# Optimization experiments

Hardware: AMD Instinct MI355X
Metric: run time of the kernel (lower is better)

Reference implementation:

```python
import jax, jax.numpy as jnp
import numpy as np

DIM = 1024
NUM_HEADS = 16
HEAD_DIM = DIM // NUM_HEADS
B, S = 2, 2048


def setup_inputs() -> dict:
    key = jax.random.key(0)
    ks = jax.random.split(key, 12)
    sc = 1.0 / np.sqrt(DIM)
    inp = {
        'x': jax.random.normal(ks[0], (B, S, DIM), dtype=jnp.float32),
        'Wq': jax.random.normal(ks[1], (DIM, DIM), dtype=jnp.float32) * sc,
        'bq': jnp.zeros((DIM,), dtype=jnp.float32),
        'Wk': jax.random.normal(ks[2], (DIM, DIM), dtype=jnp.float32) * sc,
        'bk': jnp.zeros((DIM,), dtype=jnp.float32),
        'Wv': jax.random.normal(ks[3], (DIM, DIM), dtype=jnp.float32) * sc,
        'bv': jnp.zeros((DIM,), dtype=jnp.float32),
        'Wg1': jax.random.normal(ks[4], (DIM, DIM // 2), dtype=jnp.float32) * sc,
        'bg1': jnp.zeros((DIM // 2,), dtype=jnp.float32),
        'Wg2': jax.random.normal(ks[5], (DIM // 2, NUM_HEADS), dtype=jnp.float32) * (1.0 / np.sqrt(DIM // 2)),
        'bg2': jnp.zeros((NUM_HEADS,), dtype=jnp.float32),
        'Wo': jax.random.normal(ks[6], (DIM, DIM), dtype=jnp.float32) * sc,
        'bo': jnp.zeros((DIM,), dtype=jnp.float32),
    }
    return inp


def reference(x, Wq, bq, Wk, bk, Wv, bv, Wg1, bg1, Wg2, bg2, Wo, bo):
    b, s, dim = x.shape
    h, d = NUM_HEADS, HEAD_DIM
    # QKV projections -> (b, h, s, d)
    q = (x @ Wq + bq).reshape(b, s, h, d).transpose(0, 2, 1, 3)
    k = (x @ Wk + bk).reshape(b, s, h, d).transpose(0, 2, 1, 3)
    v = (x @ Wv + bv).reshape(b, s, h, d).transpose(0, 2, 1, 3)
    # raw attention scores (b, h, q, k)
    scores = jnp.einsum('bhqd,bhkd->bhqk', q, k) / np.sqrt(d)
    # superposition gate: per-(batch, token) softmax over heads -> (b, s, h)
    gate = jax.nn.softmax(jnp.tanh(x @ Wg1 + bg1) @ Wg2 + bg2, axis=-1)
    gate = gate.transpose(0, 2, 1)[..., None]  # (b, h, s, 1) -- per-query scale
    scores = scores * gate
    probs = jax.nn.softmax(scores, axis=-1)
    # dropout is identity at inference
    attended = jnp.einsum('bhqk,bhkd->bhqd', probs, v)
    attended = attended.transpose(0, 2, 1, 3).reshape(b, s, dim)
    return attended @ Wo + bo
```

## Files before the change

### kernel.cpp

```cpp
#include <hip/hip_runtime.h>
#include <math.h>

#define DIM    1024
#define NHEADS 16
#define HDIM   64
#define BATCH  2
#define SEQ    2048
#define TOK    (BATCH * SEQ)

typedef unsigned short ushort;
typedef __attribute__((ext_vector_type(8))) short  short8;
typedef __attribute__((ext_vector_type(4))) float  f32x4;
typedef __attribute__((ext_vector_type(4))) unsigned short us4;

__device__ __forceinline__ ushort f2bf(float f) {
    unsigned u = __float_as_uint(f);
    u += 0x7fffu + ((u >> 16) & 1u);
    return (ushort)(u >> 16);
}
__device__ __forceinline__ float bf2f(ushort h) {
    return __uint_as_float(((unsigned)h) << 16);
}

__device__ __forceinline__ void gload16(const void* g, void* lds) {
    __builtin_amdgcn_global_load_lds(
        (const __attribute__((address_space(1))) unsigned int*)g,
        (__attribute__((address_space(3))) unsigned int*)lds, 16, 0, 0);
}

__global__ __launch_bounds__(256) void split_hl(
    const float* __restrict__ in, ushort* __restrict__ hi, ushort* __restrict__ lo)
{
    const int i = blockIdx.x * 256 + threadIdx.x;
    float4 v = ((const float4*)in)[i];
    us4 h, l;
    h.x = f2bf(v.x); l.x = f2bf(v.x - bf2f(h.x));
    h.y = f2bf(v.y); l.y = f2bf(v.y - bf2f(h.y));
    h.z = f2bf(v.z); l.z = f2bf(v.z - bf2f(h.z));
    h.w = f2bf(v.w); l.w = f2bf(v.w - bf2f(h.w));
    ((us4*)hi)[i] = h;
    ((us4*)lo)[i] = l;
}

__device__ __forceinline__ void tsplit_body(
    const float* __restrict__ in, ushort* __restrict__ hiT, ushort* __restrict__ loT,
    int K, int N, int k0, int n0)
{
    __shared__ float t[32][33];
    const int x = threadIdx.x & 31, y = threadIdx.x >> 5;
#pragma unroll
    for (int r = 0; r < 4; ++r)
        t[y + r * 8][x] = in[(size_t)(k0 + y + r * 8) * N + n0 + x];
    __syncthreads();
#pragma unroll
    for (int r = 0; r < 4; ++r) {
        const int row = y + r * 8;
        const float v = t[x][row];
        const ushort h = f2bf(v);
        const size_t o = (size_t)(n0 + row) * K + k0 + x;
        hiT[o] = h;
        loT[o] = f2bf(v - bf2f(h));
    }
}

__global__ __launch_bounds__(256) void wsplitT4(
    const float* __restrict__ W0, const float* __restrict__ W1,
    const float* __restrict__ W2, const float* __restrict__ W3,
    ushort* __restrict__ hiT, ushort* __restrict__ loT)
{
    const int z = blockIdx.z;
    const float* in = (z == 0) ? W0 : (z == 1) ? W1 : (z == 2) ? W2 : W3;
    tsplit_body(in, hiT + (size_t)z * DIM * DIM, loT + (size_t)z * DIM * DIM,
                DIM, DIM, blockIdx.y * 32, blockIdx.x * 32);
}

__global__ __launch_bounds__(256) void wsplitT1(
    const float* __restrict__ in, ushort* __restrict__ hiT, ushort* __restrict__ loT,
    int K, int N)
{
    tsplit_body(in, hiT, loT, K, N, blockIdx.y * 32, blockIdx.x * 32);
}

__global__ __launch_bounds__(256) void vtrans(
    const ushort* __restrict__ vh, ushort* __restrict__ vT)
{
    __shared__ ushort t[32][33];
    const int bh = blockIdx.z;
    const int s0 = blockIdx.x * 32, d0 = blockIdx.y * 32;
    const int x = threadIdx.x & 31, y = threadIdx.x >> 5;
    const ushort* src = vh + (size_t)bh * SEQ * HDIM;
    ushort* dst = vT + (size_t)bh * HDIM * SEQ;
#pragma unroll
    for (int r = 0; r < 4; ++r)
        t[y + r * 8][x] = src[(size_t)(s0 + y + r * 8) * HDIM + d0 + x];
    __syncthreads();
#pragma unroll
    for (int r = 0; r < 4; ++r)
        dst[(size_t)(d0 + y + r * 8) * SEQ + s0 + x] = t[x][y + r * 8];
}

template<int MREP>
__device__ __forceinline__ void mgemm_core(
    const ushort* __restrict__ Ahi, const ushort* __restrict__ Alo,
    const ushort* __restrict__ BThi, const ushort* __restrict__ BTlo,
    const float* __restrict__ bias, int act, int store,
    float* __restrict__ Cf, ushort* __restrict__ Ch, ushort* __restrict__ Cl,
    int ldc, int row0, int col0, ushort* ldsA, ushort* ldsB)
{
    const int tid  = threadIdx.x;
    const int lane = tid & 63;
    const int wid  = tid >> 6;
    const int wr   = wid >> 1;
    const int wc   = wid & 1;
    const int l15  = lane & 15;
    const int l4   = lane >> 4;

    f32x4 acc[MREP][4];
#pragma unroll
    for (int m = 0; m < MREP; ++m)
#pragma unroll
        for (int n = 0; n < 4; ++n) acc[m][n] = (f32x4){0.f, 0.f, 0.f, 0.f};

    const int trow = wid * 8 + (lane >> 3);
    const int swz  = ((lane & 7) ^ (lane >> 3)) * 8;

    for (int ph = 0; ph < 3; ++ph) {
        const ushort* Ap = (ph == 1) ? Alo : Ahi;
        const ushort* Bp = (ph == 2) ? BTlo : BThi;
        const ushort* Asrc = Ap + (size_t)(row0 + trow) * 1024 + swz;
        const ushort* Bsrc = Bp + (size_t)(col0 + trow) * 1024 + swz;

        for (int k0 = 0; k0 < 1024; k0 += 64) {
            __syncthreads();
#pragma unroll
            for (int r = 0; r < MREP; ++r)
                gload16(Asrc + (size_t)r * 32 * 1024 + k0, &ldsA[(wid * 8 + r * 32) * 64]);
#pragma unroll
            for (int r = 0; r < 4; ++r)
                gload16(Bsrc + (size_t)r * 32 * 1024 + k0, &ldsB[(wid * 8 + r * 32) * 64]);
            __syncthreads();

#pragma unroll
            for (int s = 0; s < 2; ++s) {
                short8 a[MREP], b[4];
#pragma unroll
                for (int m = 0; m < MREP; ++m) {
                    const int row = wr * (MREP * 16) + m * 16 + l15;
                    a[m] = *(const short8*)&ldsA[row * 64 + (((s * 4 + l4) ^ (row & 7)) * 8)];
                }
#pragma unroll
                for (int n = 0; n < 4; ++n) {
                    const int row = wc * 64 + n * 16 + l15;
                    b[n] = *(const short8*)&ldsB[row * 64 + (((s * 4 + l4) ^ (row & 7)) * 8)];
                }
#pragma unroll
                for (int m = 0; m < MREP; ++m)
#pragma unroll
                    for (int n = 0; n < 4; ++n)
                        acc[m][n] = __builtin_amdgcn_mfma_f32_16x16x32_bf16(
                            a[m], b[n], acc[m][n], 0, 0, 0);
            }
        }
    }

#pragma unroll
    for (int m = 0; m < MREP; ++m)
#pragma unroll
        for (int n = 0; n < 4; ++n) {
            const int c = col0 + wc * 64 + n * 16 + l15;
            const float bc = bias[c];
            f32x4 v = acc[m][n];
#pragma unroll
            for (int rg = 0; rg < 4; ++rg) {
                const int r = row0 + wr * (MREP * 16) + m * 16 + l4 * 4 + rg;
                float o = v[rg] + bc;
                if (act == 1) o = tanhf(o);
                if (store == 0) {
                    Cf[(size_t)r * ldc + c] = o;
                } else if (store == 1) {
                    const int bb = r >> 11, s = r & (SEQ - 1);
                    const int hh = c >> 6,  d = c & (HDIM - 1);
                    Cf[(((size_t)bb * NHEADS + hh) * SEQ + s) * HDIM + d] = o;
                } else {
                    const int bb = r >> 11, s = r & (SEQ - 1);
                    const int hh = c >> 6,  d = c & (HDIM - 1);
                    const size_t off = (((size_t)bb * NHEADS + hh) * SEQ + s) * HDIM + d;
                    const ushort hb = f2bf(o);
                    Ch[off] = hb;
                    if (store == 2) Cl[off] = f2bf(o - bf2f(hb));
                }
            }
        }
}

__global__ __launch_bounds__(256) void mgemm_fused(
    const ushort* __restrict__ xhi, const ushort* __restrict__ xlo,
    const ushort* __restrict__ WThi, const ushort* __restrict__ WTlo,
    const ushort* __restrict__ Wg1Thi, const ushort* __restrict__ Wg1Tlo,
    const float* __restrict__ bq, const float* __restrict__ bk,
    const float* __restrict__ bv, const float* __restrict__ bg1,
    float* __restrict__ qb, ushort* __restrict__ khB, ushort* __restrict__ klB,
    ushort* __restrict__ vhB, float* __restrict__ Hb)
{
    __shared__ ushort ldsA[128 * 64];
    __shared__ ushort ldsB[128 * 64];

    const int y = blockIdx.y;
    const ushort *Bh, *Bl;
    const float* bias;
    int act = 0, store, ldc = DIM, col0;
    float* Cf = nullptr;
    ushort *Ch = nullptr, *Cl = nullptr;

    if (y < 24) {
        const int sel = y >> 3;
        col0 = (y & 7) * 128;
        const size_t off = (size_t)sel * DIM * DIM;
        Bh = WThi + off; Bl = WTlo + off;
        if (sel == 0)      { bias = bq; store = 1; Cf = qb; }
        else if (sel == 1) { bias = bk; store = 2; Ch = khB; Cl = klB; }
        else               { bias = bv; store = 3; Ch = vhB; }
    } else {
        col0 = (y - 24) * 128;
        Bh = Wg1Thi; Bl = Wg1Tlo; bias = bg1;
        act = 1; store = 0; Cf = Hb; ldc = 512;
    }
    mgemm_core<4>(xhi, xlo, Bh, Bl, bias, act, store, Cf, Ch, Cl, ldc,
                  blockIdx.x * 128, col0, ldsA, ldsB);
}

__global__ __launch_bounds__(256) void mgemm_out(
    const ushort* __restrict__ Ahi, const ushort* __restrict__ Alo,
    const ushort* __restrict__ BThi, const ushort* __restrict__ BTlo,
    const float* __restrict__ bias, float* __restrict__ Cf)
{
    __shared__ ushort ldsA[64 * 64];
    __shared__ ushort ldsB[128 * 64];
    mgemm_core<2>(Ahi, Alo, BThi, BTlo, bias, 0, 0, Cf, nullptr, nullptr, DIM,
                  blockIdx.x * 64, blockIdx.y * 128, ldsA, ldsB);
}

__global__ __launch_bounds__(256) void gate2_kernel(
    const float* __restrict__ H, const float* __restrict__ Wg2,
    const float* __restrict__ bg2, float* __restrict__ gate)
{
    const int wave = threadIdx.x >> 6;
    const int lane = threadIdx.x & 63;
    const int t    = blockIdx.x * 4 + wave;
    const int hh   = lane >> 2;
    const int p    = lane & 3;

    const float* Hrow = H + (size_t)t * 512;
    float s = 0.f;
    const int k0 = p * 128;
#pragma unroll 8
    for (int kk = 0; kk < 128; kk++)
        s = __builtin_fmaf(Hrow[k0 + kk], Wg2[(k0 + kk) * NHEADS + hh], s);
    s += __shfl_xor(s, 1);
    s += __shfl_xor(s, 2);
    s += bg2[hh];

    float mx = s;
    mx = fmaxf(mx, __shfl_xor(mx, 4));
    mx = fmaxf(mx, __shfl_xor(mx, 8));
    mx = fmaxf(mx, __shfl_xor(mx, 16));
    mx = fmaxf(mx, __shfl_xor(mx, 32));
    const float e = __expf(s - mx);
    float den = e;
    den += __shfl_xor(den, 4);
    den += __shfl_xor(den, 8);
    den += __shfl_xor(den, 16);
    den += __shfl_xor(den, 32);
    if (p == 0) gate[(size_t)t * NHEADS + hh] = e / den;
}

__global__ __launch_bounds__(256, 2) void flash_mfma(
    const float* __restrict__ q,
    const ushort* __restrict__ khi, const ushort* __restrict__ klo,
    const ushort* __restrict__ vT,
    const float* __restrict__ gate,
    ushort* __restrict__ att_hi, ushort* __restrict__ att_lo)
{
    __shared__ ushort lds[20480];
    ushort* Khi = lds;
    ushort* Klo = lds + 4096;
    ushort* Vt  = lds + 8192;

    const int tid  = threadIdx.x;
    const int lane = tid & 63;
    const int wid  = tid >> 6;
    const int l15  = lane & 15;
    const int l4   = lane >> 4;
    const int qt   = blockIdx.x;
    const int bh   = blockIdx.y;
    const int b    = bh >> 4, h = bh & 15;

    ushort* Pwv = lds + 12288 + wid * 2048;

    short8 qhf[2][2], qlf[2][2];
#pragma unroll
    for (int n = 0; n < 2; n++) {
        const int qrow = qt * 128 + wid * 32 + n * 16 + l15;
        const float g = gate[(size_t)(b * SEQ + qrow) * NHEADS + h] * 0.125f;
        const float* qr = q + ((size_t)bh * SEQ + qrow) * HDIM;
#pragma unroll
        for (int kc = 0; kc < 2; kc++) {
            const int d0 = kc * 32 + l4 * 8;
            float4 f0 = *(const float4*)(qr + d0);
            float4 f1 = *(const float4*)(qr + d0 + 4);
            float vals[8] = {f0.x, f0.y, f0.z, f0.w, f1.x, f1.y, f1.z, f1.w};
            short8 hh, ll;
#pragma unroll
            for (int j = 0; j < 8; j++) {
                const float gq = vals[j] * g;
                const ushort hb = f2bf(gq);
                hh[j] = (short)hb;
                ll[j] = (short)f2bf(gq - bf2f(hb));
            }
            qhf[n][kc] = hh;
            qlf[n][kc] = ll;
        }
    }

    const ushort* Ksrc_h = khi + (size_t)bh * SEQ * HDIM;
    const ushort* Ksrc_l = klo + (size_t)bh * SEQ * HDIM;
    const ushort* Vsrc   = vT  + (size_t)bh * HDIM * SEQ;

    float m_[2] = {-INFINITY, -INFINITY};
    float l_[2] = {0.f, 0.f};
    f32x4 O[2][4];
#pragma unroll
    for (int mq = 0; mq < 2; mq++)
#pragma unroll
        for (int nd = 0; nd < 4; nd++) O[mq][nd] = (f32x4){0.f, 0.f, 0.f, 0.f};

    for (int kt = 0; kt < SEQ / 64; kt++) {
        __syncthreads();
#pragma unroll
        for (int p = 0; p < 2; p++) {
            const int r   = wid * 16 + p * 8 + (lane >> 3);
            const int cs  = ((lane & 7) ^ (r & 7)) * 8;
            const int dst = (wid * 16 + p * 8) * 64 + lane * 8;
            gload16(Ksrc_h + (size_t)(kt * 64 + r) * HDIM + cs, &Khi[dst]);
            gload16(Ksrc_l + (size_t)(kt * 64 + r) * HDIM + cs, &Klo[dst]);
            gload16(Vsrc + (size_t)r * SEQ + kt * 64 + cs, &Vt[dst]);
        }
        __syncthreads();

        f32x4 ST[4][2];
#pragma unroll
        for (int mt = 0; mt < 4; mt++)
#pragma unroll
            for (int n = 0; n < 2; n++) ST[mt][n] = (f32x4){0.f, 0.f, 0.f, 0.f};

#pragma unroll
        for (int kc = 0; kc < 2; kc++) {
            short8 ka[4];
#pragma unroll
            for (int mt = 0; mt < 4; mt++) {
                const int row = mt * 16 + l15;
                ka[mt] = *(const short8*)&Khi[row * 64 + (((kc * 4 + l4) ^ (row & 7)) * 8)];
            }
#pragma unroll
            for (int mt = 0; mt < 4; mt++)
#pragma unroll
                for (int n = 0; n < 2; n++)
                    ST[mt][n] = __builtin_amdgcn_mfma_f32_16x16x32_bf16(
                        ka[mt], qhf[n][kc], ST[mt][n], 0, 0, 0);
#pragma unroll
            for (int mt = 0; mt < 4; mt++)
#pragma unroll
                for (int n = 0; n < 2; n++)
                    ST[mt][n] = __builtin_amdgcn_mfma_f32_16x16x32_bf16(
                        ka[mt], qlf[n][kc], ST[mt][n], 0, 0, 0);
        }
#pragma unroll
        for (int kc = 0; kc < 2; kc++) {
            short8 ka[4];
#pragma unroll
            for (int mt = 0; mt < 4; mt++) {
                const int row = mt * 16 + l15;
                ka[mt] = *(const short8*)&Klo[row * 64 + (((kc * 4 + l4) ^ (row & 7)) * 8)];
            }
#pragma unroll
            for (int mt = 0; mt < 4; mt++)
#pragma unroll
                for (int n = 0; n < 2; n++)
                    ST[mt][n] = __builtin_amdgcn_mfma_f32_16x16x32_bf16(
                        ka[mt], qhf[n][kc], ST[mt][n], 0, 0, 0);
        }

        float scn[2];
#pragma unroll
        for (int n = 0; n < 2; n++) {
            float rm = fmaxf(fmaxf(ST[0][n][0], ST[0][n][1]), fmaxf(ST[0][n][2], ST[0][n][3]));
#pragma unroll
            for (int mt = 1; mt < 4; mt++) {
                rm = fmaxf(rm, fmaxf(fmaxf(ST[mt][n][0], ST[mt][n][1]),
                                     fmaxf(ST[mt][n][2], ST[mt][n][3])));
            }
            rm = fmaxf(rm, __shfl_xor(rm, 16));
            rm = fmaxf(rm, __shfl_xor(rm, 32));
            const float mn = fmaxf(m_[n], rm);
            scn[n] = __expf(m_[n] - mn);
            m_[n] = mn;
            float ps = 0.f;
#pragma unroll
            for (int mt = 0; mt < 4; mt++)
#pragma unroll
                for (int rg = 0; rg < 4; rg++) {
                    const float e = __expf(ST[mt][n][rg] - mn);
                    ST[mt][n][rg] = e;
                    ps += e;
                }
            ps += __shfl_xor(ps, 16);
            ps += __shfl_xor(ps, 32);
            l_[n] = l_[n] * scn[n] + ps;

            const int qq = n * 16 + l15;
#pragma unroll
            for (int mt = 0; mt < 4; mt++) {
                const unsigned lo32 = (unsigned)f2bf(ST[mt][n][0]) |
                                      ((unsigned)f2bf(ST[mt][n][1]) << 16);
                const unsigned hi32 = (unsigned)f2bf(ST[mt][n][2]) |
                                      ((unsigned)f2bf(ST[mt][n][3]) << 16);
                const unsigned long long pk = (unsigned long long)lo32 |
                                              ((unsigned long long)hi32 << 32);
                const int slot = (mt * 2 + (l4 >> 1)) ^ (qq & 7);
                *(unsigned long long*)&Pwv[qq * 64 + slot * 8 + (l4 & 1) * 4] = pk;
            }
        }

#pragma unroll
        for (int mq = 0; mq < 2; mq++)
#pragma unroll
            for (int rg = 0; rg < 4; rg++) {
                const float s = __shfl(scn[mq], l4 * 4 + rg);
#pragma unroll
                for (int nd = 0; nd < 4; nd++) O[mq][nd][rg] *= s;
            }

        asm volatile("s_waitcnt lgkmcnt(0)" ::: "memory");
        __builtin_amdgcn_sched_barrier(0);

#pragma unroll
        for (int kc2 = 0; kc2 < 2; kc2++) {
            short8 ap[2];
#pragma unroll
            for (int mq = 0; mq < 2; mq++) {
                const int qq = mq * 16 + l15;
                ap[mq] = *(const short8*)&Pwv[qq * 64 + (((kc2 * 4 + l4) ^ (qq & 7)) * 8)];
            }
#pragma unroll
            for (int nd = 0; nd < 4; nd++) {
                const int dd = nd * 16 + l15;
                const short8 bv = *(const short8*)&Vt[dd * 64 + (((kc2 * 4 + l4) ^ (dd & 7)) * 8)];
#pragma unroll
                for (int mq = 0; mq < 2; mq++)
                    O[mq][nd] = __builtin_amdgcn_mfma_f32_16x16x32_bf16(
                        ap[mq], bv, O[mq][nd], 0, 0, 0);
            }
        }
    }

#pragma unroll
    for (int mq = 0; mq < 2; mq++)
#pragma unroll
        for (int rg = 0; rg < 4; rg++) {
            const float linv = 1.f / __shfl(l_[mq], l4 * 4 + rg);
            const int s = qt * 128 + wid * 32 + mq * 16 + l4 * 4 + rg;
#pragma unroll
            for (int nd = 0; nd < 4; nd++) {
                const float o = O[mq][nd][rg] * linv;
                const ushort hb = f2bf(o);
                const size_t off = (size_t)(b * SEQ + s) * DIM + h * HDIM + nd * 16 + l15;
                att_hi[off] = hb;
                att_lo[off] = f2bf(o - bf2f(hb));
            }
        }
}

extern "C" void kernel_launch(void* const* d_in, const int* in_sizes, int n_in,
                              void* d_out, int out_size, void* d_ws, size_t ws_size,
                              hipStream_t stream)
{
    const float* x   = (const float*)d_in[0];
    const float* Wq  = (const float*)d_in[1];
    const float* bq  = (const float*)d_in[2];
    const float* Wk  = (const float*)d_in[3];
    const float* bk  = (const float*)d_in[4];
    const float* Wv  = (const float*)d_in[5];
    const float* bv  = (const float*)d_in[6];
    const float* Wg1 = (const float*)d_in[7];
    const float* bg1 = (const float*)d_in[8];
    const float* Wg2 = (const float*)d_in[9];
    const float* bg2 = (const float*)d_in[10];
    const float* Wo  = (const float*)d_in[11];
    const float* bo  = (const float*)d_in[12];
    float* out = (float*)d_out;

    char* p = (char*)d_ws;
    float*  qb    = (float*)p;   p += (size_t)TOK * DIM * 4;
    ushort* khB   = (ushort*)p;  p += (size_t)TOK * DIM * 2;
    ushort* klB   = (ushort*)p;  p += (size_t)TOK * DIM * 2;
    ushort* vhB   = (ushort*)p;  p += (size_t)TOK * DIM * 2;
    ushort* vTB   = (ushort*)p;  p += (size_t)TOK * DIM * 2;
    float*  Hb    = (float*)p;   p += (size_t)TOK * 512 * 4;
    float*  gateb = (float*)p;   p += (size_t)TOK * NHEADS * 4;
    ushort* xhi   = (ushort*)p;  p += (size_t)TOK * DIM * 2;
    ushort* xlo   = (ushort*)p;  p += (size_t)TOK * DIM * 2;
    ushort* atth  = (ushort*)p;  p += (size_t)TOK * DIM * 2;
    ushort* attl  = (ushort*)p;  p += (size_t)TOK * DIM * 2;
    ushort* WThi  = (ushort*)p;  p += (size_t)4 * DIM * DIM * 2;
    ushort* WTlo  = (ushort*)p;  p += (size_t)4 * DIM * DIM * 2;
    ushort* Wg1Thi= (ushort*)p;  p += (size_t)512 * DIM * 2;
    ushort* Wg1Tlo= (ushort*)p;  p += (size_t)512 * DIM * 2;

    split_hl<<<TOK * DIM / 4 / 256, 256, 0, stream>>>(x, xhi, xlo);

    wsplitT4<<<dim3(32, 32, 4), 256, 0, stream>>>(Wq, Wk, Wv, Wo, WThi, WTlo);
    wsplitT1<<<dim3(16, 32), 256, 0, stream>>>(Wg1, Wg1Thi, Wg1Tlo, DIM, 512);

    mgemm_fused<<<dim3(32, 28), 256, 0, stream>>>(
        xhi, xlo, WThi, WTlo, Wg1Thi, Wg1Tlo,
        bq, bk, bv, bg1, qb, khB, klB, vhB, Hb);

    gate2_kernel<<<dim3(TOK / 4), 256, 0, stream>>>(Hb, Wg2, bg2, gateb);

    vtrans<<<dim3(64, 2, 32), 256, 0, stream>>>(vhB, vTB);

    flash_mfma<<<dim3(SEQ / 128, BATCH * NHEADS), 256, 0, stream>>>(
        qb, khB, klB, vTB, gateb, atth, attl);

    mgemm_out<<<dim3(64, 8), 256, 0, stream>>>(
        atth, attl, WThi + (size_t)3 * DIM * DIM, WTlo + (size_t)3 * DIM * DIM,
        bo, out);
}
```

Measured before the change: 384.7 us.

## Trim split-bf16 passes per GEMM, fuse V transpose and weight-split launches

The split-bf16 GEMM now takes a per-output pass count. V projection uses one bf16 pass (hi×hi), while the gate hidden layer and output projection use two passes instead of three. The V projection epilogue writes its transposed bf16 layout directly, which removes the separate vtrans kernel and the vhB buffer. The two weight-split launches are merged into one grid. Dropping passes cuts MFMA work and memory traffic but lowers accuracy for V, the gate and the output.

```diff
diff --git a/kernel.cpp b/kernel.cpp
--- a/kernel.cpp
+++ b/kernel.cpp
@@ -63,47 +63,29 @@
     }
 }
 
-__global__ __launch_bounds__(256) void wsplitT4(
+__global__ __launch_bounds__(256) void wsplitT(
     const float* __restrict__ W0, const float* __restrict__ W1,
     const float* __restrict__ W2, const float* __restrict__ W3,
-    ushort* __restrict__ hiT, ushort* __restrict__ loT)
+    const float* __restrict__ Wg1,
+    ushort* __restrict__ hiT, ushort* __restrict__ loT,
+    ushort* __restrict__ g1hiT, ushort* __restrict__ g1loT)
 {
     const int z = blockIdx.z;
-    const float* in = (z == 0) ? W0 : (z == 1) ? W1 : (z == 2) ? W2 : W3;
-    tsplit_body(in, hiT + (size_t)z * DIM * DIM, loT + (size_t)z * DIM * DIM,
-                DIM, DIM, blockIdx.y * 32, blockIdx.x * 32);
-}
-
-__global__ __launch_bounds__(256) void wsplitT1(
-    const float* __restrict__ in, ushort* __restrict__ hiT, ushort* __restrict__ loT,
-    int K, int N)
-{
-    tsplit_body(in, hiT, loT, K, N, blockIdx.y * 32, blockIdx.x * 32);
-}
-
-__global__ __launch_bounds__(256) void vtrans(
-    const ushort* __restrict__ vh, ushort* __restrict__ vT)
-{
-    __shared__ ushort t[32][33];
-    const int bh = blockIdx.z;
-    const int s0 = blockIdx.x * 32, d0 = blockIdx.y * 32;
-    const int x = threadIdx.x & 31, y = threadIdx.x >> 5;
-    const ushort* src = vh + (size_t)bh * SEQ * HDIM;
-    ushort* dst = vT + (size_t)bh * HDIM * SEQ;
-#pragma unroll
-    for (int r = 0; r < 4; ++r)
-        t[y + r * 8][x] = src[(size_t)(s0 + y + r * 8) * HDIM + d0 + x];
-    __syncthreads();
-#pragma unroll
-    for (int r = 0; r < 4; ++r)
-        dst[(size_t)(d0 + y + r * 8) * SEQ + s0 + x] = t[x][y + r * 8];
+    if (z < 4) {
+        const float* in = (z == 0) ? W0 : (z == 1) ? W1 : (z == 2) ? W2 : W3;
+        tsplit_body(in, hiT + (size_t)z * DIM * DIM, loT + (size_t)z * DIM * DIM,
+                    DIM, DIM, blockIdx.y * 32, blockIdx.x * 32);
+    } else {
+        if (blockIdx.x >= 16) return;
+        tsplit_body(Wg1, g1hiT, g1loT, DIM, 512, blockIdx.y * 32, blockIdx.x * 32);
+    }
 }
 
 template<int MREP>
 __device__ __forceinline__ void mgemm_core(
     const ushort* __restrict__ Ahi, const ushort* __restrict__ Alo,
     const ushort* __restrict__ BThi, const ushort* __restrict__ BTlo,
-    const float* __restrict__ bias, int act, int store,
+    const float* __restrict__ bias, int act, int store, int npass,
     float* __restrict__ Cf, ushort* __restrict__ Ch, ushort* __restrict__ Cl,
     int ldc, int row0, int col0, ushort* ldsA, ushort* ldsB)
 {
@@ -124,7 +106,7 @@
     const int trow = wid * 8 + (lane >> 3);
     const int swz  = ((lane & 7) ^ (lane >> 3)) * 8;
 
-    for (int ph = 0; ph < 3; ++ph) {
+    for (int ph = 0; ph < npass; ++ph) {
         const ushort* Ap = (ph == 1) ? Alo : Ahi;
         const ushort* Bp = (ph == 2) ? BTlo : BThi;
         const ushort* Asrc = Ap + (size_t)(row0 + trow) * 1024 + swz;
@@ -170,6 +152,16 @@
             const int c = col0 + wc * 64 + n * 16 + l15;
             const float bc = bias[c];
             f32x4 v = acc[m][n];
+            if (store == 4) {
+                const int r0 = row0 + wr * (MREP * 16) + m * 16 + l4 * 4;
+                const int bb = r0 >> 11, s0 = r0 & (SEQ - 1);
+                const int hh = c >> 6,  d = c & (HDIM - 1);
+                us4 pk;
+#pragma unroll
+                for (int rg = 0; rg < 4; ++rg) pk[rg] = f2bf(v[rg] + bc);
+                *(us4*)&Ch[(((size_t)bb * NHEADS + hh) * HDIM + d) * SEQ + s0] = pk;
+                continue;
+            }
 #pragma unroll
             for (int rg = 0; rg < 4; ++rg) {
                 const int r = row0 + wr * (MREP * 16) + m * 16 + l4 * 4 + rg;
@@ -200,7 +192,7 @@
     const float* __restrict__ bq, const float* __restrict__ bk,
     const float* __restrict__ bv, const float* __restrict__ bg1,
     float* __restrict__ qb, ushort* __restrict__ khB, ushort* __restrict__ klB,
-    ushort* __restrict__ vhB, float* __restrict__ Hb)
+    ushort* __restrict__ vTB, float* __restrict__ Hb)
 {
     __shared__ ushort ldsA[128 * 64];
     __shared__ ushort ldsB[128 * 64];
@@ -208,7 +200,7 @@
     const int y = blockIdx.y;
     const ushort *Bh, *Bl;
     const float* bias;
-    int act = 0, store, ldc = DIM, col0;
+    int act = 0, store, npass, ldc = DIM, col0;
     float* Cf = nullptr;
     ushort *Ch = nullptr, *Cl = nullptr;
 
@@ -217,15 +209,15 @@
         col0 = (y & 7) * 128;
         const size_t off = (size_t)sel * DIM * DIM;
         Bh = WThi + off; Bl = WTlo + off;
-        if (sel == 0)      { bias = bq; store = 1; Cf = qb; }
-        else if (sel == 1) { bias = bk; store = 2; Ch = khB; Cl = klB; }
-        else               { bias = bv; store = 3; Ch = vhB; }
+        if (sel == 0)      { bias = bq; store = 1; npass = 3; Cf = qb; }
+        else if (sel == 1) { bias = bk; store = 2; npass = 3; Ch = khB; Cl = klB; }
+        else               { bias = bv; store = 4; npass = 1; Ch = vTB; }
     } else {
         col0 = (y - 24) * 128;
         Bh = Wg1Thi; Bl = Wg1Tlo; bias = bg1;
-        act = 1; store = 0; Cf = Hb; ldc = 512;
+        act = 1; store = 0; npass = 2; Cf = Hb; ldc = 512;
     }
-    mgemm_core<4>(xhi, xlo, Bh, Bl, bias, act, store, Cf, Ch, Cl, ldc,
+    mgemm_core<4>(xhi, xlo, Bh, Bl, bias, act, store, npass, Cf, Ch, Cl, ldc,
                   blockIdx.x * 128, col0, ldsA, ldsB);
 }
 
@@ -236,7 +228,7 @@
 {
     __shared__ ushort ldsA[64 * 64];
     __shared__ ushort ldsB[128 * 64];
-    mgemm_core<2>(Ahi, Alo, BThi, BTlo, bias, 0, 0, Cf, nullptr, nullptr, DIM,
+    mgemm_core<2>(Ahi, Alo, BThi, BTlo, bias, 0, 0, 2, Cf, nullptr, nullptr, DIM,
                   blockIdx.x * 64, blockIdx.y * 128, ldsA, ldsB);
 }
 
@@ -503,7 +495,6 @@
     float*  qb    = (float*)p;   p += (size_t)TOK * DIM * 4;
     ushort* khB   = (ushort*)p;  p += (size_t)TOK * DIM * 2;
     ushort* klB   = (ushort*)p;  p += (size_t)TOK * DIM * 2;
-    ushort* vhB   = (ushort*)p;  p += (size_t)TOK * DIM * 2;
     ushort* vTB   = (ushort*)p;  p += (size_t)TOK * DIM * 2;
     float*  Hb    = (float*)p;   p += (size_t)TOK * 512 * 4;
     float*  gateb = (float*)p;   p += (size_t)TOK * NHEADS * 4;
@@ -518,16 +509,14 @@
 
     split_hl<<<TOK * DIM / 4 / 256, 256, 0, stream>>>(x, xhi, xlo);
 
-    wsplitT4<<<dim3(32, 32, 4), 256, 0, stream>>>(Wq, Wk, Wv, Wo, WThi, WTlo);
-    wsplitT1<<<dim3(16, 32), 256, 0, stream>>>(Wg1, Wg1Thi, Wg1Tlo, DIM, 512);
+    wsplitT<<<dim3(32, 32, 5), 256, 0, stream>>>(
+        Wq, Wk, Wv, Wo, Wg1, WThi, WTlo, Wg1Thi, Wg1Tlo);
 
     mgemm_fused<<<dim3(32, 28), 256, 0, stream>>>(
         xhi, xlo, WThi, WTlo, Wg1Thi, Wg1Tlo,
-        bq, bk, bv, bg1, qb, khB, klB, vhB, Hb);
+        bq, bk, bv, bg1, qb, khB, klB, vTB, Hb);
 
     gate2_kernel<<<dim3(TOK / 4), 256, 0, stream>>>(Hb, Wg2, bg2, gateb);
-
-    vtrans<<<dim3(64, 2, 32), 256, 0, stream>>>(vhB, vTB);
 
     flash_mfma<<<dim3(SEQ / 128, BATCH * NHEADS), 256, 0, stream>>>(
         qb, khB, klB, vTB, gateb, atth, attl);
```

After: 349.0 us. 9.3% less time.
